# Kernel optimization log

Hardware: AMD Instinct MI355X
Metric: run time of the kernel (lower is better)

## Reference

```python
import jax, jax.numpy as jnp
import numpy as np

B, C, W, H = 4, 256, 64, 64
CQK = max(C // 8, 1)  # 32


def setup_inputs() -> dict:
    key = jax.random.key(0)
    ks = jax.random.split(key, 7)
    s = 0.02
    return {
        "x": jax.random.normal(ks[0], (B, C, W, H), dtype=jnp.float32),
        "wq": jax.random.normal(ks[1], (CQK, C), dtype=jnp.float32) * s,
        "bq": jnp.zeros((CQK,), dtype=jnp.float32),
        "wk": jax.random.normal(ks[2], (CQK, C), dtype=jnp.float32) * s,
        "bk": jnp.zeros((CQK,), dtype=jnp.float32),
        "wv": jax.random.normal(ks[3], (C, C), dtype=jnp.float32) * s,
        "bv": jnp.zeros((C,), dtype=jnp.float32),
        "gamma": jnp.zeros((1,), dtype=jnp.float32),
    }


def reference(x, wq, bq, wk, bk, wv, bv, gamma):
    b, c, w, h = x.shape
    n = w * h
    xf = x.reshape(b, c, n)  # flatten spatial; 1x1 conv == channel matmul
    q = jnp.einsum('oc,bcn->bno', wq, xf) + bq  # (B, N, CQK)
    k = jnp.einsum('oc,bcn->bon', wk, xf) + bk[None, :, None]  # (B, CQK, N)
    energy = jnp.einsum('bno,bom->bnm', q, k)  # (B, N, N)
    attention = jax.nn.softmax(energy, axis=-1)
    v = jnp.einsum('oc,bcn->bon', wv, xf) + bv[None, :, None]  # (B, C, N)
    # out[b,c,i] = sum_j v[b,c,j] * attention[b,i,j]
    out = jnp.einsum('bcj,bij->bci', v, attention).reshape(b, c, w, h)
    out = gamma.reshape(()) * out + x
    return out, attention
```

## Files before the change

kernel.cpp:

```cpp
#include <hip/hip_runtime.h>
#include <stdint.h>

__device__ __forceinline__ float bf2f(unsigned short u) {
    return __uint_as_float(((unsigned int)u) << 16);
}
__device__ __forceinline__ unsigned short f2bf(float f) {
    unsigned int x = __float_as_uint(f);
    x += 0x7fffu + ((x >> 16) & 1u);
    return (unsigned short)(x >> 16);
}

template<bool F32>
__device__ __forceinline__ float ld_elem(const void* p, size_t i) {
    if (F32) return ((const float*)p)[i];
    return bf2f(((const unsigned short*)p)[i]);
}

typedef short bf16x8 __attribute__((ext_vector_type(8)));
typedef float f32x4  __attribute__((ext_vector_type(4)));

__global__ void detect_dtype(const void* xbuf, int nscan, int* flag) {
    const unsigned short* u = (const unsigned short*)xbuf;
    int t = threadIdx.x;
    bool big = false;
    for (int i = t; i < nscan; i += 64) {
        float v = fabsf(bf2f(u[i]));
        if (!(v <= 1.0e4f)) big = true;
    }
    unsigned long long m = __ballot(big);
    if (t == 0) flag[0] = (m != 0ull) ? 1 : 0;
}

template<bool F32>
__device__ void projs_body(const void* x, const void* wq, const void* bq,
                           const void* wk, const void* bk,
                           unsigned short* Qh, unsigned short* Ql,
                           unsigned short* Kh, unsigned short* Kl,
                           int C, int N,
                           float (*xs)[65], float (*wsh)[65])
{
    const int t  = threadIdx.x;
    const int b  = blockIdx.y;
    const int n0 = blockIdx.x * 64;
    const int tx = t & 15, ty = t >> 4;
    float acc[4][4] = {};

    for (int c0 = 0; c0 < C; c0 += 64) {
        #pragma unroll
        for (int m = 0; m < 16; ++m) {
            int lin = m * 256 + t;
            int row = lin >> 6, col = lin & 63;
            xs[row][col] = ld_elem<F32>(x, ((size_t)(b * C + c0 + row)) * N + n0 + col);
            int o = row & 31;
            wsh[row][col] = (row < 32) ? ld_elem<F32>(wq, (size_t)o * C + c0 + col)
                                       : ld_elem<F32>(wk, (size_t)o * C + c0 + col);
        }
        __syncthreads();
        #pragma unroll 8
        for (int cc = 0; cc < 64; ++cc) {
            float xv0 = xs[cc][tx*4+0], xv1 = xs[cc][tx*4+1];
            float xv2 = xs[cc][tx*4+2], xv3 = xs[cc][tx*4+3];
            #pragma unroll
            for (int rr = 0; rr < 4; ++rr) {
                float wv = wsh[ty*4+rr][cc];
                acc[rr][0] = fmaf(wv, xv0, acc[rr][0]);
                acc[rr][1] = fmaf(wv, xv1, acc[rr][1]);
                acc[rr][2] = fmaf(wv, xv2, acc[rr][2]);
                acc[rr][3] = fmaf(wv, xv3, acc[rr][3]);
            }
        }
        __syncthreads();
    }

    unsigned short* sb = (unsigned short*)&xs[0][0];
    #pragma unroll
    for (int rr = 0; rr < 4; ++rr) {
        int r = ty*4 + rr;
        int o = r & 31;
        float bias = (r < 32) ? ld_elem<F32>(bq, o) : ld_elem<F32>(bk, o);
        int ah = (r < 32) ? 0 : 2;
        #pragma unroll
        for (int c = 0; c < 4; ++c) {
            float f = acc[rr][c] + bias;
            unsigned short h = f2bf(f);
            float rem = f - bf2f(h);
            unsigned short l = f2bf(rem);
            int n = tx*4 + c;
            sb[(ah    ) * 2048 + n * 32 + o] = h;
            sb[(ah + 1) * 2048 + n * 32 + o] = l;
        }
    }
    __syncthreads();
    {
        int n  = t >> 2;
        int ch = (t & 3) * 8;
        size_t gofs = ((size_t)(b * N + n0 + n)) * 32 + ch;
        int    lofs = n * 32 + ch;
        *(uint4*)(Qh + gofs) = *(const uint4*)(sb + 0*2048 + lofs);
        *(uint4*)(Ql + gofs) = *(const uint4*)(sb + 1*2048 + lofs);
        *(uint4*)(Kh + gofs) = *(const uint4*)(sb + 2*2048 + lofs);
        *(uint4*)(Kl + gofs) = *(const uint4*)(sb + 3*2048 + lofs);
    }
}

__global__ __launch_bounds__(256) void proj_qk_split(
    const void* x, const void* wq, const void* bq,
    const void* wk, const void* bk, const int* flag,
    unsigned short* Qh, unsigned short* Ql,
    unsigned short* Kh, unsigned short* Kl, int C, int N)
{
    __shared__ float xs[64][65];
    __shared__ float wsh[64][65];
    if (flag[0]) projs_body<true >(x,wq,bq,wk,bk,Qh,Ql,Kh,Kl,C,N,xs,wsh);
    else         projs_body<false>(x,wq,bq,wk,bk,Qh,Ql,Kh,Kl,C,N,xs,wsh);
}

template<int NT>
__global__ __launch_bounds__(1024) void energy_softmax_mfma(
    const unsigned short* __restrict__ Qh, const unsigned short* __restrict__ Ql,
    const unsigned short* __restrict__ Kh, const unsigned short* __restrict__ Kl,
    void* outbase, const int* __restrict__ flag, size_t outElems, int N)
{
    __shared__ float redm[16][16];
    __shared__ float reds[16][16];
    const int t    = threadIdx.x;
    const int wave = t >> 6, lane = t & 63;
    const int lr   = lane & 15, lk = lane >> 4;
    const int b    = blockIdx.y;
    const int i0   = blockIdx.x * 16;

    const size_t qoff = ((size_t)(b * N + i0 + lr)) * 32 + lk * 8;
    bf16x8 qh = *(const bf16x8*)(Qh + qoff);
    bf16x8 ql = *(const bf16x8*)(Ql + qoff);

    const int j0 = wave * NT * 16;
    const size_t koff = ((size_t)(b * N + j0 + lr)) * 32 + lk * 8;

    f32x4 acc[NT];
    #pragma unroll
    for (int k = 0; k < NT; ++k) {
        bf16x8 kh = *(const bf16x8*)(Kh + koff + (size_t)k * 512);
        bf16x8 kl = *(const bf16x8*)(Kl + koff + (size_t)k * 512);
        f32x4 a = {0.f, 0.f, 0.f, 0.f};
        a = __builtin_amdgcn_mfma_f32_16x16x32_bf16(qh, kh, a, 0, 0, 0);
        a = __builtin_amdgcn_mfma_f32_16x16x32_bf16(ql, kh, a, 0, 0, 0);
        a = __builtin_amdgcn_mfma_f32_16x16x32_bf16(qh, kl, a, 0, 0, 0);
        acc[k] = a;
    }

    float m[4];
    #pragma unroll
    for (int r = 0; r < 4; ++r) {
        float v = acc[0][r];
        #pragma unroll
        for (int k = 1; k < NT; ++k) v = fmaxf(v, acc[k][r]);
        v = fmaxf(v, __shfl_xor(v, 1, 64));
        v = fmaxf(v, __shfl_xor(v, 2, 64));
        v = fmaxf(v, __shfl_xor(v, 4, 64));
        v = fmaxf(v, __shfl_xor(v, 8, 64));
        m[r] = v;
    }
    if (lr == 0) {
        #pragma unroll
        for (int r = 0; r < 4; ++r) redm[wave][lk*4 + r] = m[r];
    }
    __syncthreads();
    #pragma unroll
    for (int r = 0; r < 4; ++r) {
        float v = redm[0][lk*4 + r];
        #pragma unroll
        for (int w = 1; w < 16; ++w) v = fmaxf(v, redm[w][lk*4 + r]);
        m[r] = v;
    }

    float s[4] = {0.f, 0.f, 0.f, 0.f};
    #pragma unroll
    for (int k = 0; k < NT; ++k) {
        #pragma unroll
        for (int r = 0; r < 4; ++r) {
            float e = __expf(acc[k][r] - m[r]);
            acc[k][r] = e;
            s[r] += e;
        }
    }
    #pragma unroll
    for (int r = 0; r < 4; ++r) {
        float v = s[r];
        v += __shfl_xor(v, 1, 64);
        v += __shfl_xor(v, 2, 64);
        v += __shfl_xor(v, 4, 64);
        v += __shfl_xor(v, 8, 64);
        s[r] = v;
    }
    if (lr == 0) {
        #pragma unroll
        for (int r = 0; r < 4; ++r) reds[wave][lk*4 + r] = s[r];
    }
    __syncthreads();
    #pragma unroll
    for (int r = 0; r < 4; ++r) {
        float v = 0.f;
        #pragma unroll
        for (int w = 0; w < 16; ++w) v += reds[w][lk*4 + r];
        s[r] = 1.0f / v;
    }

    if (flag[0]) {
        float* att = (float*)((char*)outbase + outElems * 4u);
        #pragma unroll
        for (int r = 0; r < 4; ++r) {
            float* rp = att + ((size_t)(b * N + i0 + lk*4 + r)) * N + j0 + lr;
            #pragma unroll
            for (int k = 0; k < NT; ++k)
                __builtin_nontemporal_store(acc[k][r] * s[r], rp + k * 16);
        }
    } else {
        unsigned short* att = (unsigned short*)((char*)outbase + outElems * 2u);
        #pragma unroll
        for (int r = 0; r < 4; ++r) {
            unsigned short* rp = att + ((size_t)(b * N + i0 + lk*4 + r)) * N + j0 + lr;
            #pragma unroll
            for (int k = 0; k < NT; ++k)
                __builtin_nontemporal_store(f2bf(acc[k][r] * s[r]), rp + k * 16);
        }
    }
}

template<bool F32>
__device__ void proj_body(const void* x, const void* wq, const void* bq,
                          const void* wk, const void* bk,
                          float* Qt, float* Kt, int C, int N, int CQK,
                          float (*xs)[65], float (*wsh)[65])
{
    const int t  = threadIdx.x;
    const int b  = blockIdx.y;
    const int n0 = blockIdx.x * 64;
    const int tx = t & 15, ty = t >> 4;
    float acc[4][4] = {};

    for (int c0 = 0; c0 < C; c0 += 64) {
        #pragma unroll
        for (int m = 0; m < 16; ++m) {
            int lin = m * 256 + t;
            int row = lin >> 6, col = lin & 63;
            int n = n0 + col;
            xs[row][col] = (n < N)
                ? ld_elem<F32>(x, ((size_t)(b * C + c0 + row)) * N + n) : 0.f;
            int o = (row < 32) ? row : row - 32;
            float wval = 0.f;
            if (o < CQK)
                wval = (row < 32) ? ld_elem<F32>(wq, (size_t)o * C + c0 + col)
                                  : ld_elem<F32>(wk, (size_t)o * C + c0 + col);
            wsh[row][col] = wval;
        }
        __syncthreads();
        #pragma unroll 8
        for (int cc = 0; cc < 64; ++cc) {
            float xv0 = xs[cc][tx*4+0], xv1 = xs[cc][tx*4+1];
            float xv2 = xs[cc][tx*4+2], xv3 = xs[cc][tx*4+3];
            #pragma unroll
            for (int rr = 0; rr < 4; ++rr) {
                float wv = wsh[ty*4+rr][cc];
                acc[rr][0] = fmaf(wv, xv0, acc[rr][0]);
                acc[rr][1] = fmaf(wv, xv1, acc[rr][1]);
                acc[rr][2] = fmaf(wv, xv2, acc[rr][2]);
                acc[rr][3] = fmaf(wv, xv3, acc[rr][3]);
            }
        }
        __syncthreads();
    }
    #pragma unroll
    for (int rr = 0; rr < 4; ++rr) {
        int r = ty*4 + rr;
        int o = (r < 32) ? r : r - 32;
        if (o >= CQK) continue;
        float bias = (r < 32) ? ld_elem<F32>(bq, o) : ld_elem<F32>(bk, o);
        float* dst = ((r < 32) ? Qt : Kt) + ((size_t)(b * CQK + o)) * N + n0 + tx*4;
        if (n0 + 64 <= N) {
            *(float4*)dst = make_float4(acc[rr][0]+bias, acc[rr][1]+bias,
                                        acc[rr][2]+bias, acc[rr][3]+bias);
        } else {
            #pragma unroll
            for (int c = 0; c < 4; ++c)
                if (n0 + tx*4 + c < N) dst[c] = acc[rr][c] + bias;
        }
    }
}

__global__ __launch_bounds__(256) void proj_qk(
    const void* x, const void* wq, const void* bq,
    const void* wk, const void* bk, const int* flag,
    float* Qt, float* Kt, int C, int N, int CQK)
{
    __shared__ float xs[64][65];
    __shared__ float wsh[64][65];
    if (flag[0]) proj_body<true >(x,wq,bq,wk,bk,Qt,Kt,C,N,CQK,xs,wsh);
    else         proj_body<false>(x,wq,bq,wk,bk,Qt,Kt,C,N,CQK,xs,wsh);
}

template<bool F32>
__device__ void projn_body(const void* x, const void* wq, const void* bq,
                           const void* wk, const void* bk,
                           float* Qt, float* Kt, int B, int C, int N, int CQK)
{
    size_t total = (size_t)B * CQK * N;
    size_t idx = (size_t)blockIdx.x * 256 + threadIdx.x;
    bool isK = idx >= total;
    if (isK) idx -= total;
    if (idx >= total) return;
    int n = (int)(idx % N);
    size_t bo = idx / N;
    int o = (int)(bo % CQK);
    int b = (int)(bo / CQK);
    const void* w = isK ? wk : wq;
    float s = ld_elem<F32>(isK ? bk : bq, o);
    for (int c = 0; c < C; ++c)
        s = fmaf(ld_elem<F32>(w, (size_t)o * C + c),
                 ld_elem<F32>(x, ((size_t)(b * C + c)) * N + n), s);
    (isK ? Kt : Qt)[((size_t)(b * CQK + o)) * N + n] = s;
}

__global__ __launch_bounds__(256) void proj_qk_naive(
    const void* x, const void* wq, const void* bq,
    const void* wk, const void* bk, const int* flag,
    float* Qt, float* Kt, int B, int C, int N, int CQK)
{
    if (flag[0]) projn_body<true >(x,wq,bq,wk,bk,Qt,Kt,B,C,N,CQK);
    else         projn_body<false>(x,wq,bq,wk,bk,Qt,Kt,B,C,N,CQK);
}

template<int JJ>
__global__ __launch_bounds__(256) void energy_softmax_t(
    const float* __restrict__ Qt, const float* __restrict__ Kt,
    void* outbase, const int* flag, size_t outElems, int N, int CQK)
{
    __shared__ float Qs[4][64];
    __shared__ float redbuf[4][4];
    const bool f32 = flag[0] != 0;
    const int t  = threadIdx.x;
    const int b  = blockIdx.y;
    const int i0 = blockIdx.x * 4;

    for (int idx = t; idx < 4 * CQK; idx += 256) {
        int ii = idx / CQK, o = idx - ii * CQK;
        Qs[ii][o] = Qt[((size_t)(b * CQK + o)) * N + i0 + ii];
    }
    __syncthreads();

    float acc[4][JJ];
    #pragma unroll
    for (int ii = 0; ii < 4; ++ii)
        #pragma unroll
        for (int jj = 0; jj < JJ; ++jj) acc[ii][jj] = 0.f;

    const int jbase = t * JJ;
    const float* kbase = Kt + (size_t)b * CQK * N + jbase;
    #pragma unroll 4
    for (int o = 0; o < CQK; ++o) {
        const float* kp = kbase + (size_t)o * N;
        float kv[JJ];
        #pragma unroll
        for (int jj = 0; jj < JJ; jj += 4) {
            float4 kk = *(const float4*)(kp + jj);
            kv[jj+0] = kk.x; kv[jj+1] = kk.y; kv[jj+2] = kk.z; kv[jj+3] = kk.w;
        }
        float qv[4] = {Qs[0][o], Qs[1][o], Qs[2][o], Qs[3][o]};
        #pragma unroll
        for (int ii = 0; ii < 4; ++ii)
            #pragma unroll
            for (int jj = 0; jj < JJ; ++jj)
                acc[ii][jj] = fmaf(qv[ii], kv[jj], acc[ii][jj]);
    }

    const int wave = t >> 6;
    const int lane = t & 63;

    float m[4];
    #pragma unroll
    for (int ii = 0; ii < 4; ++ii) {
        float v = acc[ii][0];
        #pragma unroll
        for (int jj = 1; jj < JJ; ++jj) v = fmaxf(v, acc[ii][jj]);
        #pragma unroll
        for (int off = 32; off > 0; off >>= 1)
            v = fmaxf(v, __shfl_xor(v, off, 64));
        m[ii] = v;
    }
    if (lane == 0) {
        #pragma unroll
        for (int ii = 0; ii < 4; ++ii) redbuf[ii][wave] = m[ii];
    }
    __syncthreads();
    #pragma unroll
    for (int ii = 0; ii < 4; ++ii)
        m[ii] = fmaxf(fmaxf(redbuf[ii][0], redbuf[ii][1]),
                      fmaxf(redbuf[ii][2], redbuf[ii][3]));
    __syncthreads();

    float s[4];
    #pragma unroll
    for (int ii = 0; ii < 4; ++ii) {
        float loc = 0.f;
        #pragma unroll
        for (int jj = 0; jj < JJ; ++jj) {
            float e = __expf(acc[ii][jj] - m[ii]);
            acc[ii][jj] = e;
            loc += e;
        }
        #pragma unroll
        for (int off = 32; off > 0; off >>= 1)
            loc += __shfl_xor(loc, off, 64);
        s[ii] = loc;
    }
    if (lane == 0) {
        #pragma unroll
        for (int ii = 0; ii < 4; ++ii) redbuf[ii][wave] = s[ii];
    }
    __syncthreads();
    #pragma unroll
    for (int ii = 0; ii < 4; ++ii)
        s[ii] = (redbuf[ii][0] + redbuf[ii][1]) + (redbuf[ii][2] + redbuf[ii][3]);

    if (f32) {
        float* att = (float*)((char*)outbase + outElems * 4u);
        #pragma unroll
        for (int ii = 0; ii < 4; ++ii) {
            float r = 1.0f / s[ii];
            size_t rowoff = ((size_t)(b * N + i0 + ii)) * N + jbase;
            #pragma unroll
            for (int jj = 0; jj < JJ; jj += 4)
                *(float4*)(att + rowoff + jj) =
                    make_float4(acc[ii][jj+0]*r, acc[ii][jj+1]*r,
                                acc[ii][jj+2]*r, acc[ii][jj+3]*r);
        }
    } else {
        unsigned short* att = (unsigned short*)((char*)outbase + outElems * 2u);
        #pragma unroll
        for (int ii = 0; ii < 4; ++ii) {
            float r = 1.0f / s[ii];
            size_t rowoff = ((size_t)(b * N + i0 + ii)) * N + jbase;
            #pragma unroll
            for (int jj = 0; jj < JJ; jj += 4) {
                uint2 u;
                u.x = f2bf(acc[ii][jj+0]*r) | ((unsigned)f2bf(acc[ii][jj+1]*r) << 16);
                u.y = f2bf(acc[ii][jj+2]*r) | ((unsigned)f2bf(acc[ii][jj+3]*r) << 16);
                *(uint2*)(att + rowoff + jj) = u;
            }
        }
    }
}

__global__ __launch_bounds__(256) void energy_softmax_gen(
    const float* __restrict__ Qt, const float* __restrict__ Kt,
    void* outbase, const int* flag, size_t outElems, int N, int CQK)
{
    __shared__ float Qs[256];
    __shared__ float msh[256], ssh[256];
    const bool f32 = flag[0] != 0;
    const int t = threadIdx.x;
    const int b = blockIdx.y;
    const int i = blockIdx.x;
    for (int o = t; o < CQK && o < 256; o += 256)
        Qs[o] = Qt[((size_t)(b * CQK + o)) * N + i];
    __syncthreads();
    const float* kb = Kt + (size_t)b * CQK * N;
    float m = -3.0e38f, s = 0.f;
    for (int j = t; j < N; j += 256) {
        float e = 0.f;
        for (int o = 0; o < CQK; ++o) e = fmaf(Qs[o], kb[(size_t)o * N + j], e);
        float nm = fmaxf(m, e);
        s = s * __expf(m - nm) + __expf(e - nm);
        m = nm;
    }
    msh[t] = m; ssh[t] = s;
    __syncthreads();
    for (int off = 128; off > 0; off >>= 1) {
        if (t < off) {
            float m1 = msh[t], s1 = ssh[t];
            float m2 = msh[t+off], s2 = ssh[t+off];
            float nm, ns;
            if (s1 == 0.f)      { nm = m2; ns = s2; }
            else if (s2 == 0.f) { nm = m1; ns = s1; }
            else { nm = fmaxf(m1, m2);
                   ns = s1 * __expf(m1 - nm) + s2 * __expf(m2 - nm); }
            msh[t] = nm; ssh[t] = ns;
        }
        __syncthreads();
    }
    m = msh[0];
    float inv = 1.0f / ssh[0];
    for (int j = t; j < N; j += 256) {
        float e = 0.f;
        for (int o = 0; o < CQK; ++o) e = fmaf(Qs[o], kb[(size_t)o * N + j], e);
        float a = __expf(e - m) * inv;
        size_t idx = ((size_t)(b * N + i)) * N + j;
        if (f32) ((float*)((char*)outbase + outElems * 4u))[idx] = a;
        else ((unsigned short*)((char*)outbase + outElems * 2u))[idx] = f2bf(a);
    }
}

__global__ __launch_bounds__(256) void out_final(
    const void* x, const void* gamma, const void* wv, const void* bv,
    void* outbase, const int* flag, int B, int C, int N)
{
    const bool f32 = flag[0] != 0;
    const size_t nelem = (size_t)B * C * N;
    const float g = f32 ? ((const float*)gamma)[0]
                        : bf2f(((const unsigned short*)gamma)[0]);
    if (g == 0.0f) {
        size_t totalBytes = nelem * (f32 ? 4u : 2u);
        size_t off = ((size_t)blockIdx.x * 256 + threadIdx.x) * 16;
        if (off + 16 <= totalBytes) {
            *(uint4*)((char*)outbase + off) = *(const uint4*)((const char*)x + off);
        } else if (off < totalBytes) {
            for (size_t p = off; p < totalBytes; ++p)
                ((char*)outbase)[p] = ((const char*)x)[p];
        }
        return;
    }
    size_t cn = (size_t)C * N;
    size_t stride = (size_t)gridDim.x * 256;
    for (size_t e = (size_t)blockIdx.x * 256 + threadIdx.x; e < nelem; e += stride) {
        int b = (int)(e / cn);
        size_t r = e - (size_t)b * cn;
        int c = (int)(r / N);
        int i = (int)(r - (size_t)c * N);
        float ssum = 0.f;
        for (int j = 0; j < N; ++j) {
            float v;
            if (f32) {
                v = ((const float*)bv)[c];
                for (int cp = 0; cp < C; ++cp)
                    v = fmaf(((const float*)wv)[c * C + cp],
                             ((const float*)x)[((size_t)(b * C + cp)) * N + j], v);
                float a = ((const float*)((char*)outbase + nelem * 4u))
                              [((size_t)(b * N + i)) * N + j];
                ssum = fmaf(v, a, ssum);
            } else {
                v = bf2f(((const unsigned short*)bv)[c]);
                for (int cp = 0; cp < C; ++cp)
                    v = fmaf(bf2f(((const unsigned short*)wv)[c * C + cp]),
                             bf2f(((const unsigned short*)x)[((size_t)(b * C + cp)) * N + j]), v);
                float a = bf2f(((const unsigned short*)((char*)outbase + nelem * 2u))
                              [((size_t)(b * N + i)) * N + j]);
                ssum = fmaf(v, a, ssum);
            }
        }
        if (f32) ((float*)outbase)[e] = g * ssum + ((const float*)x)[e];
        else {
            float xe = bf2f(((const unsigned short*)x)[e]);
            ((unsigned short*)outbase)[e] = f2bf(g * ssum + xe);
        }
    }
}

extern "C" void kernel_launch(void* const* d_in, const int* in_sizes, int n_in,
                              void* d_out, int out_size, void* d_ws, size_t ws_size,
                              hipStream_t stream)
{
    int B = 4, C = 256, N = 4096, CQK = 32;
    if (n_in >= 8) {
        long long c = in_sizes[6], cqk = in_sizes[2], s0 = in_sizes[0];
        if (c > 0 && cqk > 0 &&
            in_sizes[1] == cqk * c && in_sizes[3] == cqk * c &&
            in_sizes[4] == cqk && in_sizes[5] == c * c &&
            s0 > 0 && s0 % c == 0) {
            long long bn = s0 / c;
            long long rem = (long long)out_size - s0;
            if (bn > 0 && rem > 0 && rem % bn == 0) {
                long long n = rem / bn;
                if (n > 0 && bn % n == 0) {
                    long long bb = bn / n;
                    if (bb >= 1 && bb * n * n == rem && bb * c * n == s0) {
                        B = (int)bb; N = (int)n; C = (int)c; CQK = (int)cqk;
                    }
                }
            }
        }
    }

    const void* x  = d_in[0];
    const void* wq = d_in[1];
    const void* bq = d_in[2];
    const void* wk = d_in[3];
    const void* bk = d_in[4];
    const void* wv = d_in[5];
    const void* bv = d_in[6];
    const void* gm = d_in[7];

    int* flag = (int*)d_ws;
    size_t nelem = (size_t)B * C * N;

    int nscan = in_sizes[0] < 8192 ? in_sizes[0] : 8192;
    detect_dtype<<<1, 64, 0, stream>>>(x, nscan, flag);

    bool fast = ((C % 64) == 0) && (CQK == 32) &&
                (N == 1024 || N == 2048 || N == 4096);
    unsigned short* Qh = nullptr;
    size_t perArr = (size_t)B * N * 32;
    if (fast) {
        size_t needBytes = 256 + perArr * 2 * 4;
        if (ws_size >= needBytes)
            Qh = (unsigned short*)((char*)d_ws + 256);
        else if (C >= 128)
            Qh = (unsigned short*)d_out;
        else
            fast = false;
    }

    if (fast) {
        unsigned short* Ql = Qh + perArr;
        unsigned short* Kh = Qh + 2 * perArr;
        unsigned short* Kl = Qh + 3 * perArr;
        proj_qk_split<<<dim3(N / 64, B), 256, 0, stream>>>(
            x, wq, bq, wk, bk, flag, Qh, Ql, Kh, Kl, C, N);
        dim3 eg(N / 16, B);
        if (N == 4096)
            energy_softmax_mfma<16><<<eg, 1024, 0, stream>>>(Qh, Ql, Kh, Kl, d_out, flag, nelem, N);
        else if (N == 2048)
            energy_softmax_mfma< 8><<<eg, 1024, 0, stream>>>(Qh, Ql, Kh, Kl, d_out, flag, nelem, N);
        else
            energy_softmax_mfma< 4><<<eg, 1024, 0, stream>>>(Qh, Ql, Kh, Kl, d_out, flag, nelem, N);
    } else {
        size_t stageFloats = (size_t)2 * B * CQK * N;
        float* Qt;
        if (ws_size >= 256 + stageFloats * sizeof(float))
            Qt = (float*)((char*)d_ws + 256);
        else
            Qt = (float*)d_out;
        float* Kt = Qt + (size_t)B * CQK * N;

        if ((C % 64) == 0 && CQK <= 32) {
            proj_qk<<<dim3((N + 63) / 64, B), 256, 0, stream>>>(
                x, wq, bq, wk, bk, flag, Qt, Kt, C, N, CQK);
        } else {
            size_t tot2 = (size_t)2 * B * CQK * N;
            proj_qk_naive<<<dim3((unsigned)((tot2 + 255) / 256)), 256, 0, stream>>>(
                x, wq, bq, wk, bk, flag, Qt, Kt, B, C, N, CQK);
        }

        if (CQK <= 64 && N == 1024)
            energy_softmax_t<4><<<dim3(N/4, B), 256, 0, stream>>>(Qt, Kt, d_out, flag, nelem, N, CQK);
        else if (CQK <= 64 && N == 2048)
            energy_softmax_t<8><<<dim3(N/4, B), 256, 0, stream>>>(Qt, Kt, d_out, flag, nelem, N, CQK);
        else if (CQK <= 64 && N == 4096)
            energy_softmax_t<16><<<dim3(N/4, B), 256, 0, stream>>>(Qt, Kt, d_out, flag, nelem, N, CQK);
        else
            energy_softmax_gen<<<dim3(N, B), 256, 0, stream>>>(Qt, Kt, d_out, flag, nelem, N, CQK);
    }

    size_t maxBytes = nelem * 4;
    out_final<<<dim3((unsigned)((maxBytes + 4095) / 4096)), 256, 0, stream>>>(
        x, gm, wv, bv, d_out, flag, B, C, N);
}
```

Before: 432.5 us.

## Fuse residual copy into projection and vectorize attention stores via transposed MFMA

The projection kernel now writes x into the output while it loads it, so out_final can exit early when gamma is zero instead of re-copying x. The energy MFMA operands are swapped so each lane holds four consecutive columns of one row. That allows 16-byte (fp32) or 8-byte (bf16) nontemporal vector stores of the large attention matrix and single-value row reductions. The change relies on gamma==0 for the skip path, though it checks gamma at runtime, and it adds scattered scalar stores inside the projection load loop.

```diff
diff --git a/kernel.cpp b/kernel.cpp
--- a/kernel.cpp
+++ b/kernel.cpp
@@ -18,6 +18,7 @@
 
 typedef short bf16x8 __attribute__((ext_vector_type(8)));
 typedef float f32x4  __attribute__((ext_vector_type(4)));
+typedef unsigned int u32x2 __attribute__((ext_vector_type(2)));
 
 __global__ void detect_dtype(const void* xbuf, int nscan, int* flag) {
     const unsigned short* u = (const unsigned short*)xbuf;
@@ -36,7 +37,7 @@
                            const void* wk, const void* bk,
                            unsigned short* Qh, unsigned short* Ql,
                            unsigned short* Kh, unsigned short* Kl,
-                           int C, int N,
+                           int C, int N, void* outb, int docopy,
                            float (*xs)[65], float (*wsh)[65])
 {
     const int t  = threadIdx.x;
@@ -50,7 +51,13 @@
         for (int m = 0; m < 16; ++m) {
             int lin = m * 256 + t;
             int row = lin >> 6, col = lin & 63;
-            xs[row][col] = ld_elem<F32>(x, ((size_t)(b * C + c0 + row)) * N + n0 + col);
+            size_t e = ((size_t)(b * C + c0 + row)) * N + n0 + col;
+            float xv = ld_elem<F32>(x, e);
+            xs[row][col] = xv;
+            if (docopy) {
+                if (F32) ((float*)outb)[e] = xv;
+                else     ((unsigned short*)outb)[e] = f2bf(xv);
+            }
             int o = row & 31;
             wsh[row][col] = (row < 32) ? ld_elem<F32>(wq, (size_t)o * C + c0 + col)
                                        : ld_elem<F32>(wk, (size_t)o * C + c0 + col);
@@ -107,12 +114,13 @@
     const void* x, const void* wq, const void* bq,
     const void* wk, const void* bk, const int* flag,
     unsigned short* Qh, unsigned short* Ql,
-    unsigned short* Kh, unsigned short* Kl, int C, int N)
+    unsigned short* Kh, unsigned short* Kl, int C, int N,
+    void* outb, int docopy)
 {
     __shared__ float xs[64][65];
     __shared__ float wsh[64][65];
-    if (flag[0]) projs_body<true >(x,wq,bq,wk,bk,Qh,Ql,Kh,Kl,C,N,xs,wsh);
-    else         projs_body<false>(x,wq,bq,wk,bk,Qh,Ql,Kh,Kl,C,N,xs,wsh);
+    if (flag[0]) projs_body<true >(x,wq,bq,wk,bk,Qh,Ql,Kh,Kl,C,N,outb,docopy,xs,wsh);
+    else         projs_body<false>(x,wq,bq,wk,bk,Qh,Ql,Kh,Kl,C,N,outb,docopy,xs,wsh);
 }
 
 template<int NT>
@@ -142,86 +150,63 @@
         bf16x8 kh = *(const bf16x8*)(Kh + koff + (size_t)k * 512);
         bf16x8 kl = *(const bf16x8*)(Kl + koff + (size_t)k * 512);
         f32x4 a = {0.f, 0.f, 0.f, 0.f};
-        a = __builtin_amdgcn_mfma_f32_16x16x32_bf16(qh, kh, a, 0, 0, 0);
-        a = __builtin_amdgcn_mfma_f32_16x16x32_bf16(ql, kh, a, 0, 0, 0);
-        a = __builtin_amdgcn_mfma_f32_16x16x32_bf16(qh, kl, a, 0, 0, 0);
+        a = __builtin_amdgcn_mfma_f32_16x16x32_bf16(kh, qh, a, 0, 0, 0);
+        a = __builtin_amdgcn_mfma_f32_16x16x32_bf16(kh, ql, a, 0, 0, 0);
+        a = __builtin_amdgcn_mfma_f32_16x16x32_bf16(kl, qh, a, 0, 0, 0);
         acc[k] = a;
     }
 
-    float m[4];
-    #pragma unroll
-    for (int r = 0; r < 4; ++r) {
-        float v = acc[0][r];
-        #pragma unroll
-        for (int k = 1; k < NT; ++k) v = fmaxf(v, acc[k][r]);
-        v = fmaxf(v, __shfl_xor(v, 1, 64));
-        v = fmaxf(v, __shfl_xor(v, 2, 64));
-        v = fmaxf(v, __shfl_xor(v, 4, 64));
-        v = fmaxf(v, __shfl_xor(v, 8, 64));
-        m[r] = v;
-    }
-    if (lr == 0) {
-        #pragma unroll
-        for (int r = 0; r < 4; ++r) redm[wave][lk*4 + r] = m[r];
-    }
-    __syncthreads();
-    #pragma unroll
-    for (int r = 0; r < 4; ++r) {
-        float v = redm[0][lk*4 + r];
-        #pragma unroll
-        for (int w = 1; w < 16; ++w) v = fmaxf(v, redm[w][lk*4 + r]);
-        m[r] = v;
-    }
-
-    float s[4] = {0.f, 0.f, 0.f, 0.f};
+    float m = acc[0][0];
     #pragma unroll
     for (int k = 0; k < NT; ++k) {
         #pragma unroll
+        for (int r = 0; r < 4; ++r) m = fmaxf(m, acc[k][r]);
+    }
+    m = fmaxf(m, __shfl_xor(m, 16, 64));
+    m = fmaxf(m, __shfl_xor(m, 32, 64));
+    if (lane < 16) redm[wave][lr] = m;
+    __syncthreads();
+    #pragma unroll
+    for (int w = 0; w < 16; ++w) m = fmaxf(m, redm[w][lr]);
+
+    float s = 0.f;
+    #pragma unroll
+    for (int k = 0; k < NT; ++k) {
+        #pragma unroll
         for (int r = 0; r < 4; ++r) {
-            float e = __expf(acc[k][r] - m[r]);
+            float e = __expf(acc[k][r] - m);
             acc[k][r] = e;
-            s[r] += e;
-        }
-    }
-    #pragma unroll
-    for (int r = 0; r < 4; ++r) {
-        float v = s[r];
-        v += __shfl_xor(v, 1, 64);
-        v += __shfl_xor(v, 2, 64);
-        v += __shfl_xor(v, 4, 64);
-        v += __shfl_xor(v, 8, 64);
-        s[r] = v;
-    }
-    if (lr == 0) {
-        #pragma unroll
-        for (int r = 0; r < 4; ++r) reds[wave][lk*4 + r] = s[r];
-    }
-    __syncthreads();
-    #pragma unroll
-    for (int r = 0; r < 4; ++r) {
-        float v = 0.f;
-        #pragma unroll
-        for (int w = 0; w < 16; ++w) v += reds[w][lk*4 + r];
-        s[r] = 1.0f / v;
-    }
+            s += e;
+        }
+    }
+    s += __shfl_xor(s, 16, 64);
+    s += __shfl_xor(s, 32, 64);
+    if (lane < 16) reds[wave][lr] = s;
+    __syncthreads();
+    s = 0.f;
+    #pragma unroll
+    for (int w = 0; w < 16; ++w) s += reds[w][lr];
+    const float rs = 1.0f / s;
 
     if (flag[0]) {
         float* att = (float*)((char*)outbase + outElems * 4u);
-        #pragma unroll
-        for (int r = 0; r < 4; ++r) {
-            float* rp = att + ((size_t)(b * N + i0 + lk*4 + r)) * N + j0 + lr;
-            #pragma unroll
-            for (int k = 0; k < NT; ++k)
-                __builtin_nontemporal_store(acc[k][r] * s[r], rp + k * 16);
+        float* rp  = att + ((size_t)(b * N + i0 + lr)) * N + j0 + lk * 4;
+        #pragma unroll
+        for (int k = 0; k < NT; ++k) {
+            f32x4 v;
+            v[0] = acc[k][0] * rs; v[1] = acc[k][1] * rs;
+            v[2] = acc[k][2] * rs; v[3] = acc[k][3] * rs;
+            __builtin_nontemporal_store(v, (f32x4*)(rp + k * 16));
         }
     } else {
         unsigned short* att = (unsigned short*)((char*)outbase + outElems * 2u);
-        #pragma unroll
-        for (int r = 0; r < 4; ++r) {
-            unsigned short* rp = att + ((size_t)(b * N + i0 + lk*4 + r)) * N + j0 + lr;
-            #pragma unroll
-            for (int k = 0; k < NT; ++k)
-                __builtin_nontemporal_store(f2bf(acc[k][r] * s[r]), rp + k * 16);
+        unsigned short* rp  = att + ((size_t)(b * N + i0 + lr)) * N + j0 + lk * 4;
+        #pragma unroll
+        for (int k = 0; k < NT; ++k) {
+            u32x2 u;
+            u[0] = (unsigned)f2bf(acc[k][0]*rs) | ((unsigned)f2bf(acc[k][1]*rs) << 16);
+            u[1] = (unsigned)f2bf(acc[k][2]*rs) | ((unsigned)f2bf(acc[k][3]*rs) << 16);
+            __builtin_nontemporal_store(u, (u32x2*)(rp + k * 16));
         }
     }
 }
@@ -501,13 +486,14 @@
 
 __global__ __launch_bounds__(256) void out_final(
     const void* x, const void* gamma, const void* wv, const void* bv,
-    void* outbase, const int* flag, int B, int C, int N)
+    void* outbase, const int* flag, int B, int C, int N, int precopied)
 {
     const bool f32 = flag[0] != 0;
     const size_t nelem = (size_t)B * C * N;
     const float g = f32 ? ((const float*)gamma)[0]
                         : bf2f(((const unsigned short*)gamma)[0]);
     if (g == 0.0f) {
+        if (precopied) return;
         size_t totalBytes = nelem * (f32 ? 4u : 2u);
         size_t off = ((size_t)blockIdx.x * 256 + threadIdx.x) * 16;
         if (off + 16 <= totalBytes) {
@@ -597,15 +583,18 @@
     bool fast = ((C % 64) == 0) && (CQK == 32) &&
                 (N == 1024 || N == 2048 || N == 4096);
     unsigned short* Qh = nullptr;
+    int stagingInWs = 0;
     size_t perArr = (size_t)B * N * 32;
     if (fast) {
         size_t needBytes = 256 + perArr * 2 * 4;
-        if (ws_size >= needBytes)
+        if (ws_size >= needBytes) {
             Qh = (unsigned short*)((char*)d_ws + 256);
-        else if (C >= 128)
+            stagingInWs = 1;
+        } else if (C >= 128) {
             Qh = (unsigned short*)d_out;
-        else
+        } else {
             fast = false;
+        }
     }
 
     if (fast) {
@@ -613,7 +602,7 @@
         unsigned short* Kh = Qh + 2 * perArr;
         unsigned short* Kl = Qh + 3 * perArr;
         proj_qk_split<<<dim3(N / 64, B), 256, 0, stream>>>(
-            x, wq, bq, wk, bk, flag, Qh, Ql, Kh, Kl, C, N);
+            x, wq, bq, wk, bk, flag, Qh, Ql, Kh, Kl, C, N, d_out, stagingInWs);
         dim3 eg(N / 16, B);
         if (N == 4096)
             energy_softmax_mfma<16><<<eg, 1024, 0, stream>>>(Qh, Ql, Kh, Kl, d_out, flag, nelem, N);
@@ -651,5 +640,5 @@
 
     size_t maxBytes = nelem * 4;
     out_final<<<dim3((unsigned)((maxBytes + 4095) / 4096)), 256, 0, stream>>>(
-        x, gm, wv, bv, d_out, flag, B, C, N);
-}
+        x, gm, wv, bv, d_out, flag, B, C, N, fast ? stagingInWs : 0);
+}
```

New measurement: 419.0 us. 3.1% less time.
